# Performance work log

Hardware: AMD Instinct MI355X
Metric: run time of the kernel (lower is better)

Reference implementation:

```python
import jax, jax.numpy as jnp
import numpy as np


def _l2norm(t, eps=1e-12):
    # matches torch F.normalize(p=2, dim=-1): x / max(||x||_2, eps)
    n = jnp.sqrt(jnp.sum(t * t, axis=-1, keepdims=True))
    return t / jnp.maximum(n, eps)


def setup_inputs() -> dict:
    key = jax.random.key(0)
    ks = jax.random.split(key, 8)
    B, N, C, H, W = 16, 4, 256, 64, 64
    d = 64  # dim_head
    x = jax.random.normal(ks[0], (B, C, H, W), jnp.float32)
    fmaps = jax.random.normal(ks[1], (B, N, C, H, W), jnp.float32)
    Wq = jax.random.normal(ks[2], (N * d, C), jnp.float32) * 0.02   # Linear [out,in]
    Wk = jax.random.normal(ks[3], (N, d, C), jnp.float32) * 0.02    # grouped 1x1 conv, per-group [d,C]
    Wv = jax.random.normal(ks[4], (N, d, C), jnp.float32) * 0.02
    rescale = jnp.ones((N, 1, 1), jnp.float32)
    Wffn = jax.random.normal(ks[5], (C, N * d), jnp.float32) * 0.02
    bffn = jnp.zeros((C,), jnp.float32)
    return {"x": x, "fmaps": fmaps, "Wq": Wq, "Wk": Wk, "Wv": Wv,
            "rescale": rescale, "Wffn": Wffn, "bffn": bffn}


def reference(x, fmaps, Wq, Wk, Wv, rescale, Wffn, bffn):
    B, N, C, H, W = fmaps.shape
    d = Wk.shape[1]
    HW = H * W

    # x: [B,C,H,W] -> tokens [B,HW,C]
    x_in = jnp.transpose(x, (0, 2, 3, 1)).reshape(B, HW, C)
    q_in = jnp.einsum('bsc,oc->bso', x_in, Wq)            # [B,HW,N*d]

    # grouped 1x1 convs on fmaps (group = fmap index n)
    fm = fmaps.reshape(B, N, C, HW)                       # [B,N,C,HW]
    k = jnp.einsum('bncs,ndc->bnds', fm, Wk)              # [B,N,d,HW]
    v = jnp.einsum('bncs,ndc->bnds', fm, Wv)              # [B,N,d,HW]

    q = jnp.transpose(q_in.reshape(B, HW, N, d), (0, 2, 3, 1))  # [B,N,d,HW]

    qn = _l2norm(q)   # normalize over spatial (HW) axis
    kn = _l2norm(k)

    attn = jnp.einsum('bnds,bnes->bnde', kn, qn) * rescale      # [B,N,d,d]
    attn = jax.nn.softmax(attn, axis=-1)
    out = jnp.einsum('bnde,bnes->bnds', attn, v)                # [B,N,d,HW]

    out = jnp.transpose(out, (0, 3, 1, 2)).reshape(B, HW, N * d)  # [B,HW,N*d]
    out = out + q_in
    out = jnp.einsum('bsi,ci->bsc', out, Wffn) + bffn + q_in      # ffn + residual
    return jnp.transpose(out.reshape(B, H, W, C), (0, 3, 1, 2))   # [B,C,H,W]
```

## Files before the change

kernel.cpp:

```cpp
#include <hip/hip_runtime.h>
#include <hip/hip_bf16.h>
#include <cmath>

using bf16 = __hip_bfloat16;
typedef __attribute__((ext_vector_type(4))) float  f32x4;
typedef __attribute__((ext_vector_type(8))) short  bf16x8;
typedef unsigned int u32;
typedef unsigned short u16;

__device__ __forceinline__ void gl_lds16(const bf16* g, bf16* l) {
    __builtin_amdgcn_global_load_lds(
        (const __attribute__((address_space(1))) u32*)g,
        (__attribute__((address_space(3))) u32*)l, 16, 0, 0);
}
__device__ __forceinline__ u32 pk2(float a, float b) {
    bf16 ha = __float2bfloat16(a), hb = __float2bfloat16(b);
    return (u32)*(u16*)&ha | ((u32)*(u16*)&hb << 16);
}
__device__ __forceinline__ float b2f(u16 v) {
    return __uint_as_float((u32)v << 16);
}

__global__ __launch_bounds__(256) void wconv(
    const float* __restrict__ a, const float* __restrict__ b,
    const float* __restrict__ c, const float* __restrict__ d,
    bf16* __restrict__ o)
{
    int i = blockIdx.x * 256 + threadIdx.x;
    int which = i >> 16, off = i & 65535;
    const float* s = (which == 0) ? a : (which == 1) ? b : (which == 2) ? c : d;
    o[i] = __float2bfloat16(s[off]);
}

__global__ __launch_bounds__(256) void wqf_kernel(
    const float* __restrict__ Wffn, const float* __restrict__ Wq,
    bf16* __restrict__ WQF)
{
    const int c = blockIdx.x, cp = threadIdx.x;
    float acc = Wq[c * 256 + cp];
#pragma unroll 8
    for (int i = 0; i < 256; ++i)
        acc += Wffn[c * 256 + i] * Wq[i * 256 + cp];
    WQF[c * 256 + cp] = __float2bfloat16(acc);
}

__global__ __launch_bounds__(512) void qproj8(
    const float* __restrict__ x,
    const bf16* __restrict__ Wq,
    bf16* __restrict__ qch,
    bf16* __restrict__ xbf)
{
    __shared__ bf16 sW[256 * 64];
    __shared__ bf16 sX[128 * 72];
    const int t = threadIdx.x;
    const int lane = t & 63, wid = t >> 6;
    const int wm = wid >> 1, wn = wid & 1;
    const int g = lane >> 4, lr = lane & 15;
    const int s0 = blockIdx.x * 128;
    const int b = blockIdx.y;
    const float* xb = x + (long)b * 1048576;
    bf16* xob = xbf + (long)b * 1048576;

    f32x4 acc[4][4];
#pragma unroll
    for (int i = 0; i < 4; ++i)
#pragma unroll
        for (int j = 0; j < 4; ++j) acc[i][j] = (f32x4){0.f, 0.f, 0.f, 0.f};

    const int p  = t & 31;
    const int sl = t >> 5;

    for (int c0 = 0; c0 < 256; c0 += 64) {
        __syncthreads();
#pragma unroll
        for (int i = 0; i < 4; ++i) {
            int lin = i * 512 + t, r = lin >> 3, ch = lin & 7;
            gl_lds16(Wq + (long)r * 256 + c0 + ((ch ^ (r & 7)) << 3), &sW[lin * 8]);
        }
#pragma unroll
        for (int j = 0; j < 2; ++j) {
            int s4 = j * 16 + sl;
            const float* src = xb + (long)(c0 + 2 * p) * 4096 + s0 + s4 * 4;
            float4 a = *(const float4*)src;
            float4 bq = *(const float4*)(src + 4096);
            u32 w0 = pk2(a.x, bq.x), w1 = pk2(a.y, bq.y);
            u32 w2 = pk2(a.z, bq.z), w3 = pk2(a.w, bq.w);
            char* base = (char*)sX + p * 4 + (s4 * 4) * 144;
            *(u32*)(base +   0) = w0;
            *(u32*)(base + 144) = w1;
            *(u32*)(base + 288) = w2;
            *(u32*)(base + 432) = w3;
            long xo = (long)(s0 + s4 * 4) * 256 + c0 + 2 * p;
            *(u32*)(xob + xo)       = w0;
            *(u32*)(xob + xo + 256) = w1;
            *(u32*)(xob + xo + 512) = w2;
            *(u32*)(xob + xo + 768) = w3;
        }
        __syncthreads();
#pragma unroll
        for (int kk = 0; kk < 2; ++kk) {
            bf16x8 aw[4], fx[4];
#pragma unroll
            for (int mf = 0; mf < 4; ++mf) {
                int r = wm * 64 + mf * 16 + lr;
                aw[mf] = *(const bf16x8*)((const char*)sW + r * 128 + (((kk * 4 + g) ^ (r & 7)) << 4));
            }
#pragma unroll
            for (int nf = 0; nf < 4; ++nf) {
                int s = wn * 64 + nf * 16 + lr;
                fx[nf] = *(const bf16x8*)((const char*)sX + s * 144 + (kk * 4 + g) * 16);
            }
#pragma unroll
            for (int mf = 0; mf < 4; ++mf)
#pragma unroll
                for (int nf = 0; nf < 4; ++nf)
                    acc[mf][nf] = __builtin_amdgcn_mfma_f32_16x16x32_bf16(
                        aw[mf], fx[nf], acc[mf][nf], 0, 0, 0);
        }
    }
    bf16* qb = qch + (long)b * 1048576;
#pragma unroll
    for (int mf = 0; mf < 4; ++mf)
#pragma unroll
        for (int nf = 0; nf < 4; ++nf)
#pragma unroll
            for (int e = 0; e < 4; ++e) {
                int o = wm * 64 + mf * 16 + g * 4 + e;
                int s = s0 + wn * 64 + nf * 16 + lr;
                qb[(long)o * 4096 + s] = __float2bfloat16(acc[mf][nf][e]);
            }
}

__global__ __launch_bounds__(256) void kvqk(
    const float* __restrict__ fm,
    const bf16* __restrict__ Wk,
    const bf16* __restrict__ Wv,
    const bf16* __restrict__ qch,
    bf16* __restrict__ vT,
    float* __restrict__ part,
    float* __restrict__ sums)
{
    __shared__ bf16 sF[128 * 72];
    __shared__ bf16 sWk[64 * 64];
    __shared__ bf16 sWv[64 * 64];
    __shared__ bf16 sKt[64 * 128];
    __shared__ bf16 sQ[64 * 128];
    const int t = threadIdx.x;
    const int lane = t & 63, wid = t >> 6;
    const int g = lane >> 4, lr = lane & 15;
    const int ch_ = blockIdx.x;
    const int bn = blockIdx.y, n = bn & 3;
    const float* fb = fm + (long)bn * 1048576;
    const bf16* WkN = Wk + (long)n * 16384;
    const bf16* WvN = Wv + (long)n * 16384;
    const bf16* qbase = qch + (long)bn * 262144;
    bf16* vtb = vT + (long)bn * 262144;

    const int p  = t & 31;
    const int sl = t >> 5;
    const int srow = t >> 1, shalf = t & 1;

    f32x4 accQ[4];
#pragma unroll
    for (int i = 0; i < 4; ++i) accQ[i] = (f32x4){0.f, 0.f, 0.f, 0.f};
    float ssum = 0.f;

    for (int sub = 0; sub < 4; ++sub) {
        const int ss0 = ch_ * 512 + sub * 128;
        f32x4 acc1[4][2], acc2[2][4];
#pragma unroll
        for (int i = 0; i < 4; ++i)
#pragma unroll
            for (int j = 0; j < 2; ++j) {
                acc1[i][j] = (f32x4){0.f, 0.f, 0.f, 0.f};
                acc2[j][i] = (f32x4){0.f, 0.f, 0.f, 0.f};
            }

        for (int c0 = 0; c0 < 256; c0 += 64) {
            __syncthreads();
#pragma unroll
            for (int i = 0; i < 2; ++i) {
                int lin = i * 256 + t, r = lin >> 3, c = lin & 7;
                int off = r * 256 + c0 + ((c ^ (r & 7)) << 3);
                gl_lds16(WkN + off, &sWk[lin * 8]);
                gl_lds16(WvN + off, &sWv[lin * 8]);
            }
#pragma unroll
            for (int j = 0; j < 4; ++j) {
                int s4 = j * 8 + sl;
                const float* src = fb + (long)(c0 + 2 * p) * 4096 + ss0 + s4 * 4;
                float4 a = *(const float4*)src;
                float4 bq = *(const float4*)(src + 4096);
                char* base = (char*)sF + p * 4 + (s4 * 4) * 144;
                *(u32*)(base +   0) = pk2(a.x, bq.x);
                *(u32*)(base + 144) = pk2(a.y, bq.y);
                *(u32*)(base + 288) = pk2(a.z, bq.z);
                *(u32*)(base + 432) = pk2(a.w, bq.w);
            }
            __syncthreads();
#pragma unroll
            for (int kk = 0; kk < 2; ++kk) {
                bf16x8 ak[4], ff[2], bv[4];
#pragma unroll
                for (int mf = 0; mf < 4; ++mf) {
                    int r = mf * 16 + lr;
                    ak[mf] = *(const bf16x8*)((const char*)sWk + r * 128 + (((kk * 4 + g) ^ (r & 7)) << 4));
                }
#pragma unroll
                for (int i = 0; i < 2; ++i) {
                    int s = wid * 32 + i * 16 + lr;
                    ff[i] = *(const bf16x8*)((const char*)sF + s * 144 + (kk * 4 + g) * 16);
                }
#pragma unroll
                for (int nf = 0; nf < 4; ++nf) {
                    int r = nf * 16 + lr;
                    bv[nf] = *(const bf16x8*)((const char*)sWv + r * 128 + (((kk * 4 + g) ^ (r & 7)) << 4));
                }
#pragma unroll
                for (int mf = 0; mf < 4; ++mf)
#pragma unroll
                    for (int i = 0; i < 2; ++i)
                        acc1[mf][i] = __builtin_amdgcn_mfma_f32_16x16x32_bf16(
                            ak[mf], ff[i], acc1[mf][i], 0, 0, 0);
#pragma unroll
                for (int i = 0; i < 2; ++i)
#pragma unroll
                    for (int nf = 0; nf < 4; ++nf)
                        acc2[i][nf] = __builtin_amdgcn_mfma_f32_16x16x32_bf16(
                            ff[i], bv[nf], acc2[i][nf], 0, 0, 0);
            }
        }
#pragma unroll
        for (int i = 0; i < 4; ++i) {
            int lin = i * 256 + t, r = lin >> 4, c = lin & 15;
            gl_lds16(qbase + (long)r * 4096 + ss0 + ((c ^ (r & 7)) << 3), &sQ[lin * 8]);
        }
#pragma unroll
        for (int i = 0; i < 2; ++i)
#pragma unroll
            for (int nf = 0; nf < 4; ++nf)
#pragma unroll
                for (int e = 0; e < 4; ++e) {
                    int s = ss0 + wid * 32 + i * 16 + g * 4 + e;
                    vtb[(long)s * 64 + nf * 16 + lr] = __float2bfloat16(acc2[i][nf][e]);
                }
#pragma unroll
        for (int mf = 0; mf < 4; ++mf)
#pragma unroll
            for (int i = 0; i < 2; ++i)
#pragma unroll
                for (int e = 0; e < 4; ++e) {
                    int dd = mf * 16 + g * 4 + e;
                    int sc = wid * 32 + i * 16 + lr;
                    bf16 hv = __float2bfloat16(acc1[mf][i][e]);
                    int byte = (dd * 256 + sc * 2) ^ ((dd & 7) << 4);
                    *(u16*)((char*)sKt + byte) = *(u16*)&hv;
                }
        __syncthreads();
#pragma unroll
        for (int kks = 0; kks < 4; ++kks) {
            int rA = wid * 16 + lr;
            bf16x8 af = *(const bf16x8*)((const char*)sKt + rA * 256 + (((kks * 4 + g) ^ (rA & 7)) << 4));
            bf16x8 bq[4];
#pragma unroll
            for (int nf = 0; nf < 4; ++nf) {
                int rB = nf * 16 + lr;
                bq[nf] = *(const bf16x8*)((const char*)sQ + rB * 256 + (((kks * 4 + g) ^ (rB & 7)) << 4));
            }
#pragma unroll
            for (int nf = 0; nf < 4; ++nf)
                accQ[nf] = __builtin_amdgcn_mfma_f32_16x16x32_bf16(
                    af, bq[nf], accQ[nf], 0, 0, 0);
        }
        {
            const char* base = (srow < 64) ? (const char*)sKt + srow * 256
                                           : (const char*)sQ + (srow - 64) * 256;
            int r7 = srow & 7;
#pragma unroll
            for (int j = 0; j < 8; ++j) {
                bf16x8 v = *(const bf16x8*)(base + (((shalf * 8 + j) ^ r7) << 4));
#pragma unroll
                for (int e = 0; e < 8; ++e) {
                    float f = b2f((u16)v[e]);
                    ssum += f * f;
                }
            }
        }
    }
    float* pp = part + ((long)bn * 8 + ch_) * 4096;
#pragma unroll
    for (int nf = 0; nf < 4; ++nf)
#pragma unroll
        for (int e = 0; e < 4; ++e) {
            int dd = wid * 16 + g * 4 + e;
            pp[dd * 64 + nf * 16 + lr] = accQ[nf][e];
        }
    ssum += __shfl_xor(ssum, 1);
    if (shalf == 0) {
        if (srow < 64) atomicAdd(&sums[4096 + bn * 64 + srow], ssum);
        else           atomicAdd(&sums[bn * 64 + (srow - 64)], ssum);
    }
}

__global__ __launch_bounds__(256) void finalizeM2(
    const float* __restrict__ part, const float* __restrict__ sums,
    const float* __restrict__ rescale, const bf16* __restrict__ Wf,
    bf16* __restrict__ M2)
{
    __shared__ float att[64][65];
    __shared__ float rmax[64], rsm[64], iq[64], ik[64];
    __shared__ bf16 sWf[256 * 64];
    __shared__ bf16 attT[64 * 64];
    const int bn = blockIdx.x, n = bn & 3, b = bn >> 2;
    const int t = threadIdx.x;
    const int lane = t & 63, wid = t >> 6;
    const int g = lane >> 4, lr = lane & 15;
    const float rs = rescale[n];

#pragma unroll
    for (int i = 0; i < 8; ++i) {
        int lin = i * 256 + t, r = lin >> 3, c = lin & 7;
        gl_lds16(Wf + (long)r * 256 + n * 64 + ((c ^ (r & 7)) << 3), &sWf[lin * 8]);
    }
    if (t < 64)        ik[t]      = 1.f / fmaxf(sqrtf(sums[4096 + bn * 64 + t]), 1e-12f);
    else if (t < 128)  iq[t - 64] = 1.f / fmaxf(sqrtf(sums[bn * 64 + t - 64]), 1e-12f);
    __syncthreads();

    const float* pb = part + (long)bn * 8 * 4096;
#pragma unroll
    for (int p_ = 0; p_ < 16; ++p_) {
        int lin = p_ * 256 + t;
        int dd = lin >> 6, e = lin & 63;
        float v = 0.f;
#pragma unroll
        for (int c = 0; c < 8; ++c) v += pb[c * 4096 + lin];
        att[dd][e] = v * ik[dd] * iq[e] * rs;
    }
    __syncthreads();
    if (t < 64) {
        float m = -1e30f;
        for (int e = 0; e < 64; ++e) m = fmaxf(m, att[t][e]);
        float sm = 0.f;
        for (int e = 0; e < 64; ++e) sm += expf(att[t][e] - m);
        rmax[t] = m;
        rsm[t] = 1.0f / sm;
    }
    __syncthreads();
#pragma unroll
    for (int p_ = 0; p_ < 16; ++p_) {
        int lin = p_ * 256 + t;
        int dd = lin >> 6, e = lin & 63;
        bf16 hv = __float2bfloat16(expf(att[dd][e] - rmax[dd]) * rsm[dd]);
        int byte = (e * 128 + dd * 2) ^ ((e & 7) << 4);
        *(u16*)((char*)attT + byte) = *(u16*)&hv;
    }
    __syncthreads();

    f32x4 acc[4][4];
#pragma unroll
    for (int i = 0; i < 4; ++i)
#pragma unroll
        for (int j = 0; j < 4; ++j) acc[i][j] = (f32x4){0.f, 0.f, 0.f, 0.f};
#pragma unroll
    for (int kk = 0; kk < 2; ++kk) {
        bf16x8 aw[4], bt[4];
#pragma unroll
        for (int mf = 0; mf < 4; ++mf) {
            int r = wid * 64 + mf * 16 + lr;
            aw[mf] = *(const bf16x8*)((const char*)sWf + r * 128 + (((kk * 4 + g) ^ (r & 7)) << 4));
        }
#pragma unroll
        for (int nf = 0; nf < 4; ++nf) {
            int e = nf * 16 + lr;
            bt[nf] = *(const bf16x8*)((const char*)attT + e * 128 + (((kk * 4 + g) ^ (e & 7)) << 4));
        }
#pragma unroll
        for (int mf = 0; mf < 4; ++mf)
#pragma unroll
            for (int nf = 0; nf < 4; ++nf)
                acc[mf][nf] = __builtin_amdgcn_mfma_f32_16x16x32_bf16(
                    aw[mf], bt[nf], acc[mf][nf], 0, 0, 0);
    }
    bf16* m2b = M2 + (long)b * 65536;
#pragma unroll
    for (int mf = 0; mf < 4; ++mf)
#pragma unroll
        for (int nf = 0; nf < 4; ++nf)
#pragma unroll
            for (int e = 0; e < 4; ++e) {
                int c = wid * 64 + mf * 16 + g * 4 + e;
                m2b[c * 256 + n * 64 + nf * 16 + lr] = __float2bfloat16(acc[mf][nf][e]);
            }
}

__global__ __launch_bounds__(512) void outgemm(
    const bf16* __restrict__ M2,
    const bf16* __restrict__ WQF,
    const bf16* __restrict__ vT,
    const bf16* __restrict__ xbf,
    const float* __restrict__ bffn,
    float* __restrict__ out)
{
    __shared__ bf16 sA[256 * 64];
    __shared__ bf16 sB[128 * 64];
    const int t = threadIdx.x;
    const int lane = t & 63, wid = t >> 6;
    const int wm = wid >> 1, wn = wid & 1;
    const int g = lane >> 4, lr = lane & 15;
    const int s0 = blockIdx.x * 128;
    const int b = blockIdx.y;

    f32x4 acc[4][4];
#pragma unroll
    for (int i = 0; i < 4; ++i)
#pragma unroll
        for (int j = 0; j < 4; ++j) acc[i][j] = (f32x4){0.f, 0.f, 0.f, 0.f};

    for (int ch = 0; ch < 8; ++ch) {
        const bf16* Asrc;
        const bf16* Bsrc;
        int Brs;
        if (ch < 4) {
            Asrc = M2 + (long)b * 65536 + ch * 64;
            Bsrc = vT + ((long)b * 4 + ch) * 262144 + (long)s0 * 64;
            Brs = 64;
        } else {
            Asrc = WQF + (ch - 4) * 64;
            Bsrc = xbf + (long)b * 1048576 + (long)s0 * 256 + (ch - 4) * 64;
            Brs = 256;
        }
        __syncthreads();
#pragma unroll
        for (int i = 0; i < 4; ++i) {
            int lin = i * 512 + t, r = lin >> 3, c = lin & 7;
            gl_lds16(Asrc + (long)r * 256 + ((c ^ (r & 7)) << 3), &sA[lin * 8]);
        }
#pragma unroll
        for (int i = 0; i < 2; ++i) {
            int lin = i * 512 + t, r = lin >> 3, c = lin & 7;
            gl_lds16(Bsrc + (long)r * Brs + ((c ^ (r & 7)) << 3), &sB[lin * 8]);
        }
        __syncthreads();
#pragma unroll
        for (int kk = 0; kk < 2; ++kk) {
            bf16x8 aw[4], bz[4];
#pragma unroll
            for (int mf = 0; mf < 4; ++mf) {
                int r = wm * 64 + mf * 16 + lr;
                aw[mf] = *(const bf16x8*)((const char*)sA + r * 128 + (((kk * 4 + g) ^ (r & 7)) << 4));
            }
#pragma unroll
            for (int nf = 0; nf < 4; ++nf) {
                int r = wn * 64 + nf * 16 + lr;
                bz[nf] = *(const bf16x8*)((const char*)sB + r * 128 + (((kk * 4 + g) ^ (r & 7)) << 4));
            }
#pragma unroll
            for (int mf = 0; mf < 4; ++mf)
#pragma unroll
                for (int nf = 0; nf < 4; ++nf)
                    acc[mf][nf] = __builtin_amdgcn_mfma_f32_16x16x32_bf16(
                        aw[mf], bz[nf], acc[mf][nf], 0, 0, 0);
        }
    }
    float* ob = out + (long)b * 1048576;
#pragma unroll
    for (int mf = 0; mf < 4; ++mf)
#pragma unroll
        for (int e = 0; e < 4; ++e) {
            int c = wm * 64 + mf * 16 + g * 4 + e;
            float bv = bffn[c];
#pragma unroll
            for (int nf = 0; nf < 4; ++nf) {
                int s = s0 + wn * 64 + nf * 16 + lr;
                ob[(long)c * 4096 + s] = acc[mf][nf][e] + bv;
            }
        }
}

extern "C" void kernel_launch(void* const* d_in, const int* in_sizes, int n_in,
                              void* d_out, int out_size, void* d_ws, size_t ws_size,
                              hipStream_t stream) {
    const float* x       = (const float*)d_in[0];
    const float* fmaps   = (const float*)d_in[1];
    const float* Wq      = (const float*)d_in[2];
    const float* Wk      = (const float*)d_in[3];
    const float* Wv      = (const float*)d_in[4];
    const float* rescale = (const float*)d_in[5];
    const float* Wffn    = (const float*)d_in[6];
    const float* bffn    = (const float*)d_in[7];
    float* out = (float*)d_out;

    char* w = (char*)d_ws;
    bf16* qch   = (bf16*)(w + 0);
    bf16* vT    = (bf16*)(w + 33554432L);
    bf16* xbf   = (bf16*)(w + 67108864L);
    float* part = (float*)(w + 100663296L);
    float* sums = (float*)(w + 109051904L);
    bf16* M2    = (bf16*)(w + 109084672L);
    bf16* Wq_b  = (bf16*)(w + 111181824L);
    bf16* Wk_b  = Wq_b + 65536;
    bf16* Wv_b  = Wq_b + 131072;
    bf16* Wf_b  = Wq_b + 196608;
    bf16* WQF   = (bf16*)(w + 111706112L);

    dim3 blk(256);

    hipMemsetAsync(sums, 0, 32768, stream);
    wconv<<<dim3(1024), blk, 0, stream>>>(Wq, Wk, Wv, Wffn, Wq_b);
    wqf_kernel<<<dim3(256), blk, 0, stream>>>(Wffn, Wq, WQF);
    qproj8<<<dim3(32, 16), dim3(512), 0, stream>>>(x, Wq_b, qch, xbf);
    kvqk<<<dim3(8, 64), blk, 0, stream>>>(fmaps, Wk_b, Wv_b, qch, vT, part, sums);
    finalizeM2<<<dim3(64), blk, 0, stream>>>(part, sums, rescale, Wf_b, M2);
    outgemm<<<dim3(32, 16), dim3(512), 0, stream>>>(M2, WQF, vT, xbf, bffn, out);
}
```

Measured before the change: 209.2 us.

## Merge setup kernels, stage stores through LDS, compute norms from registers

Fuses the weight conversion, WQF precompute and the sums memset into one launch, removing two launches and a memset. qproj8 and kvqk now write q and vT outputs through LDS so the global stores are coalesced 16-byte rows instead of scattered 2-byte stores. kvqk reads q fragments straight from global memory instead of staging them in LDS. The squared-norm sums are accumulated from registers (fp32 k values, bf16 q fragments) and reduced with shuffles, replacing the separate LDS re-read pass, at the cost of extra syncs and more registers.

Result: slower. 220.6 us (+5.5%).

```diff
diff --git a/kernel.cpp b/kernel.cpp
--- a/kernel.cpp
+++ b/kernel.cpp
@@ -21,27 +21,32 @@
     return __uint_as_float((u32)v << 16);
 }
 
-__global__ __launch_bounds__(256) void wconv(
-    const float* __restrict__ a, const float* __restrict__ b,
-    const float* __restrict__ c, const float* __restrict__ d,
-    bf16* __restrict__ o)
+__global__ __launch_bounds__(256) void wqfconv(
+    const float* __restrict__ Wq, const float* __restrict__ Wk,
+    const float* __restrict__ Wv, const float* __restrict__ Wffn,
+    bf16* __restrict__ Wb,
+    bf16* __restrict__ WQF,
+    float* __restrict__ sums)
 {
-    int i = blockIdx.x * 256 + threadIdx.x;
-    int which = i >> 16, off = i & 65535;
-    const float* s = (which == 0) ? a : (which == 1) ? b : (which == 2) ? c : d;
-    o[i] = __float2bfloat16(s[off]);
-}
-
-__global__ __launch_bounds__(256) void wqf_kernel(
-    const float* __restrict__ Wffn, const float* __restrict__ Wq,
-    bf16* __restrict__ WQF)
-{
-    const int c = blockIdx.x, cp = threadIdx.x;
-    float acc = Wq[c * 256 + cp];
+    const int bx = blockIdx.x, t = threadIdx.x;
+    if (bx < 256) {
+        float acc = Wq[bx * 256 + t];
 #pragma unroll 8
-    for (int i = 0; i < 256; ++i)
-        acc += Wffn[c * 256 + i] * Wq[i * 256 + cp];
-    WQF[c * 256 + cp] = __float2bfloat16(acc);
+        for (int i = 0; i < 256; ++i)
+            acc += Wffn[bx * 256 + i] * Wq[i * 256 + t];
+        WQF[bx * 256 + t] = __float2bfloat16(acc);
+    } else if (bx < 320) {
+#pragma unroll
+        for (int k = 0; k < 16; ++k) {
+            int idx = (bx - 256) * 4096 + k * 256 + t;
+            int which = idx >> 16, off = idx & 65535;
+            const float* s = (which == 0) ? Wq : (which == 1) ? Wk
+                           : (which == 2) ? Wv : Wffn;
+            Wb[idx] = __float2bfloat16(s[off]);
+        }
+    } else {
+        sums[(bx - 320) * 256 + t] = 0.f;
+    }
 }
 
 __global__ __launch_bounds__(512) void qproj8(
@@ -50,8 +55,8 @@
     bf16* __restrict__ qch,
     bf16* __restrict__ xbf)
 {
-    __shared__ bf16 sW[256 * 64];
-    __shared__ bf16 sX[128 * 72];
+    __shared__ __align__(16) bf16 sW[256 * 64];
+    __shared__ __align__(16) bf16 sX[128 * 72];
     const int t = threadIdx.x;
     const int lane = t & 63, wid = t >> 6;
     const int wm = wid >> 1, wn = wid & 1;
@@ -120,15 +125,30 @@
     }
     bf16* qb = qch + (long)b * 1048576;
 #pragma unroll
-    for (int mf = 0; mf < 4; ++mf)
-#pragma unroll
-        for (int nf = 0; nf < 4; ++nf)
-#pragma unroll
-            for (int e = 0; e < 4; ++e) {
-                int o = wm * 64 + mf * 16 + g * 4 + e;
-                int s = s0 + wn * 64 + nf * 16 + lr;
-                qb[(long)o * 4096 + s] = __float2bfloat16(acc[mf][nf][e]);
-            }
+    for (int h = 0; h < 2; ++h) {
+        __syncthreads();
+        if ((wm >> 1) == h) {
+#pragma unroll
+            for (int mf = 0; mf < 4; ++mf)
+#pragma unroll
+                for (int nf = 0; nf < 4; ++nf)
+#pragma unroll
+                    for (int e = 0; e < 4; ++e) {
+                        int ol = (wm & 1) * 64 + mf * 16 + g * 4 + e;
+                        int s = wn * 64 + nf * 16 + lr;
+                        bf16 hv = __float2bfloat16(acc[mf][nf][e]);
+                        int byte = (ol * 256 + s * 2) ^ ((ol & 7) << 4);
+                        *(u16*)((char*)sW + byte) = *(u16*)&hv;
+                    }
+        }
+        __syncthreads();
+#pragma unroll
+        for (int i = 0; i < 4; ++i) {
+            int lin = i * 512 + t, r = lin >> 4, c = lin & 15;
+            uint4 v = *(const uint4*)((const char*)sW + r * 256 + (((c ^ (r & 7))) << 4));
+            *(uint4*)(qb + (long)(h * 128 + r) * 4096 + s0 + c * 8) = v;
+        }
+    }
 }
 
 __global__ __launch_bounds__(256) void kvqk(
@@ -140,11 +160,11 @@
     float* __restrict__ part,
     float* __restrict__ sums)
 {
-    __shared__ bf16 sF[128 * 72];
-    __shared__ bf16 sWk[64 * 64];
-    __shared__ bf16 sWv[64 * 64];
-    __shared__ bf16 sKt[64 * 128];
-    __shared__ bf16 sQ[64 * 128];
+    __shared__ __align__(16) char smem[51200];
+    bf16* sF  = (bf16*)smem;
+    bf16* sWk = (bf16*)(smem + 34816);
+    bf16* sWv = (bf16*)(smem + 43008);
+
     const int t = threadIdx.x;
     const int lane = t & 63, wid = t >> 6;
     const int g = lane >> 4, lr = lane & 15;
@@ -158,12 +178,16 @@
 
     const int p  = t & 31;
     const int sl = t >> 5;
-    const int srow = t >> 1, shalf = t & 1;
 
     f32x4 accQ[4];
 #pragma unroll
     for (int i = 0; i < 4; ++i) accQ[i] = (f32x4){0.f, 0.f, 0.f, 0.f};
-    float ssum = 0.f;
+    float kss[4][4];
+#pragma unroll
+    for (int i = 0; i < 4; ++i)
+#pragma unroll
+        for (int j = 0; j < 4; ++j) kss[i][j] = 0.f;
+    float qss[4] = {0.f, 0.f, 0.f, 0.f};
 
     for (int sub = 0; sub < 4; ++sub) {
         const int ss0 = ch_ * 512 + sub * 128;
@@ -230,20 +254,7 @@
                             ff[i], bv[nf], acc2[i][nf], 0, 0, 0);
             }
         }
-#pragma unroll
-        for (int i = 0; i < 4; ++i) {
-            int lin = i * 256 + t, r = lin >> 4, c = lin & 15;
-            gl_lds16(qbase + (long)r * 4096 + ss0 + ((c ^ (r & 7)) << 3), &sQ[lin * 8]);
-        }
-#pragma unroll
-        for (int i = 0; i < 2; ++i)
-#pragma unroll
-            for (int nf = 0; nf < 4; ++nf)
-#pragma unroll
-                for (int e = 0; e < 4; ++e) {
-                    int s = ss0 + wid * 32 + i * 16 + g * 4 + e;
-                    vtb[(long)s * 64 + nf * 16 + lr] = __float2bfloat16(acc2[i][nf][e]);
-                }
+        __syncthreads();
 #pragma unroll
         for (int mf = 0; mf < 4; ++mf)
 #pragma unroll
@@ -252,39 +263,50 @@
                 for (int e = 0; e < 4; ++e) {
                     int dd = mf * 16 + g * 4 + e;
                     int sc = wid * 32 + i * 16 + lr;
-                    bf16 hv = __float2bfloat16(acc1[mf][i][e]);
+                    float f = acc1[mf][i][e];
+                    kss[mf][e] += f * f;
+                    bf16 hv = __float2bfloat16(f);
                     int byte = (dd * 256 + sc * 2) ^ ((dd & 7) << 4);
-                    *(u16*)((char*)sKt + byte) = *(u16*)&hv;
+                    *(u16*)(smem + byte) = *(u16*)&hv;
+                }
+#pragma unroll
+        for (int i = 0; i < 2; ++i)
+#pragma unroll
+            for (int nf = 0; nf < 4; ++nf)
+#pragma unroll
+                for (int e = 0; e < 4; ++e) {
+                    int slc = wid * 32 + i * 16 + g * 4 + e;
+                    int ec = nf * 16 + lr;
+                    bf16 hv = __float2bfloat16(acc2[i][nf][e]);
+                    *(u16*)(smem + 16384 + slc * 144 + ec * 2) = *(u16*)&hv;
                 }
         __syncthreads();
 #pragma unroll
         for (int kks = 0; kks < 4; ++kks) {
             int rA = wid * 16 + lr;
-            bf16x8 af = *(const bf16x8*)((const char*)sKt + rA * 256 + (((kks * 4 + g) ^ (rA & 7)) << 4));
+            bf16x8 af = *(const bf16x8*)(smem + rA * 256 + (((kks * 4 + g) ^ (rA & 7)) << 4));
             bf16x8 bq[4];
 #pragma unroll
             for (int nf = 0; nf < 4; ++nf) {
                 int rB = nf * 16 + lr;
-                bq[nf] = *(const bf16x8*)((const char*)sQ + rB * 256 + (((kks * 4 + g) ^ (rB & 7)) << 4));
-            }
-#pragma unroll
-            for (int nf = 0; nf < 4; ++nf)
+                bq[nf] = *(const bf16x8*)(qbase + (long)rB * 4096 + ss0 + (kks * 4 + g) * 8);
+            }
+#pragma unroll
+            for (int nf = 0; nf < 4; ++nf) {
                 accQ[nf] = __builtin_amdgcn_mfma_f32_16x16x32_bf16(
                     af, bq[nf], accQ[nf], 0, 0, 0);
-        }
-        {
-            const char* base = (srow < 64) ? (const char*)sKt + srow * 256
-                                           : (const char*)sQ + (srow - 64) * 256;
-            int r7 = srow & 7;
-#pragma unroll
-            for (int j = 0; j < 8; ++j) {
-                bf16x8 v = *(const bf16x8*)(base + (((shalf * 8 + j) ^ r7) << 4));
-#pragma unroll
-                for (int e = 0; e < 8; ++e) {
-                    float f = b2f((u16)v[e]);
-                    ssum += f * f;
+#pragma unroll
+                for (int e2 = 0; e2 < 8; ++e2) {
+                    float f = b2f((u16)bq[nf][e2]);
+                    qss[nf] += f * f;
                 }
             }
+        }
+#pragma unroll
+        for (int i2 = 0; i2 < 4; ++i2) {
+            int lin = i2 * 256 + t, r = lin >> 3, c = lin & 7;
+            uint4 v = *(const uint4*)(smem + 16384 + r * 144 + c * 16);
+            *(uint4*)(vtb + (long)(ss0 + r) * 64 + c * 8) = v;
         }
     }
     float* pp = part + ((long)bn * 8 + ch_) * 4096;
@@ -295,10 +317,25 @@
             int dd = wid * 16 + g * 4 + e;
             pp[dd * 64 + nf * 16 + lr] = accQ[nf][e];
         }
-    ssum += __shfl_xor(ssum, 1);
-    if (shalf == 0) {
-        if (srow < 64) atomicAdd(&sums[4096 + bn * 64 + srow], ssum);
-        else           atomicAdd(&sums[bn * 64 + (srow - 64)], ssum);
+#pragma unroll
+    for (int mf = 0; mf < 4; ++mf)
+#pragma unroll
+        for (int e = 0; e < 4; ++e) {
+            float v = kss[mf][e];
+            v += __shfl_xor(v, 1);
+            v += __shfl_xor(v, 2);
+            v += __shfl_xor(v, 4);
+            v += __shfl_xor(v, 8);
+            if (lr == 0)
+                atomicAdd(&sums[4096 + bn * 64 + mf * 16 + g * 4 + e], v);
+        }
+#pragma unroll
+    for (int nf = 0; nf < 4; ++nf) {
+        float v = qss[nf];
+        v += __shfl_xor(v, 16);
+        v += __shfl_xor(v, 32);
+        if (wid == 0 && g == 0)
+            atomicAdd(&sums[bn * 64 + nf * 16 + lr], v);
     }
 }
 
@@ -309,8 +346,8 @@
 {
     __shared__ float att[64][65];
     __shared__ float rmax[64], rsm[64], iq[64], ik[64];
-    __shared__ bf16 sWf[256 * 64];
-    __shared__ bf16 attT[64 * 64];
+    __shared__ __align__(16) bf16 sWf[256 * 64];
+    __shared__ __align__(16) bf16 attT[64 * 64];
     const int bn = blockIdx.x, n = bn & 3, b = bn >> 2;
     const int t = threadIdx.x;
     const int lane = t & 63, wid = t >> 6;
@@ -401,8 +438,8 @@
     const float* __restrict__ bffn,
     float* __restrict__ out)
 {
-    __shared__ bf16 sA[256 * 64];
-    __shared__ bf16 sB[128 * 64];
+    __shared__ __align__(16) bf16 sA[256 * 64];
+    __shared__ __align__(16) bf16 sB[128 * 64];
     const int t = threadIdx.x;
     const int lane = t & 63, wid = t >> 6;
     const int wm = wid >> 1, wn = wid & 1;
@@ -497,17 +534,16 @@
     float* part = (float*)(w + 100663296L);
     float* sums = (float*)(w + 109051904L);
     bf16* M2    = (bf16*)(w + 109084672L);
-    bf16* Wq_b  = (bf16*)(w + 111181824L);
-    bf16* Wk_b  = Wq_b + 65536;
-    bf16* Wv_b  = Wq_b + 131072;
-    bf16* Wf_b  = Wq_b + 196608;
+    bf16* Wb    = (bf16*)(w + 111181824L);
+    bf16* Wq_b  = Wb;
+    bf16* Wk_b  = Wb + 65536;
+    bf16* Wv_b  = Wb + 131072;
+    bf16* Wf_b  = Wb + 196608;
     bf16* WQF   = (bf16*)(w + 111706112L);
 
     dim3 blk(256);
 
-    hipMemsetAsync(sums, 0, 32768, stream);
-    wconv<<<dim3(1024), blk, 0, stream>>>(Wq, Wk, Wv, Wffn, Wq_b);
-    wqf_kernel<<<dim3(256), blk, 0, stream>>>(Wffn, Wq, WQF);
+    wqfconv<<<dim3(352), blk, 0, stream>>>(Wq, Wk, Wv, Wffn, Wb, WQF, sums);
     qproj8<<<dim3(32, 16), dim3(512), 0, stream>>>(x, Wq_b, qch, xbf);
     kvqk<<<dim3(8, 64), blk, 0, stream>>>(fmaps, Wk_b, Wv_b, qch, vT, part, sums);
     finalizeM2<<<dim3(64), blk, 0, stream>>>(part, sums, rescale, Wf_b, M2);
```
